# Kernel tuning notes

Measured on AMD Instinct MI355X. Metric: run time of the kernel, lower is better.

## Reference

```python
import jax, jax.numpy as jnp
import numpy as np

L = 4          # dilation_depth
HID = 32       # hidden_channels
F_IN = 16
F_OUT = 16
K = 2          # conv kernel size


def setup_inputs() -> dict:
    key = jax.random.key(0)
    ks = jax.random.split(key, 20)
    B, T, N, F = 8, 512, 128, F_IN
    s = 0.1
    inp = {
        "X": jax.random.normal(ks[0], (B, T, N, F), jnp.float32),
        "A": jax.random.normal(ks[1], (N, N), jnp.float32) / jnp.sqrt(N).astype(jnp.float32),
        "in_w": jax.random.normal(ks[2], (F, 3 * HID), jnp.float32) * s,
        "in_b": jnp.zeros((3 * HID,), jnp.float32),
        "ct_w": jax.random.normal(ks[3], (L, K, HID, HID), jnp.float32) * s,
        "ct_b": jnp.zeros((L, HID), jnp.float32),
        "cs_w": jax.random.normal(ks[4], (L, K, HID, HID), jnp.float32) * s,
        "cs_b": jnp.zeros((L, HID), jnp.float32),
        "gcn_w": jax.random.normal(ks[5], (L, HID, HID), jnp.float32) * s,
        "gcn_b": jnp.zeros((L, HID), jnp.float32),
        "res_w": jax.random.normal(ks[6], (L, HID, HID), jnp.float32) * s,
        "res_b": jnp.zeros((L, HID), jnp.float32),
        "skip_w": jax.random.normal(ks[7], (L, HID, HID), jnp.float32) * s,
        "skip_b": jnp.zeros((L, HID), jnp.float32),
        "out1_w": jax.random.normal(ks[8], (HID, HID), jnp.float32) * s,
        "out1_b": jnp.zeros((HID,), jnp.float32),
        "out2_w": jax.random.normal(ks[9], (HID, F_OUT), jnp.float32) * s,
        "out2_b": jnp.zeros((F_OUT,), jnp.float32),
    }
    return inp


def _causal_conv(x, w, b, dilation):
    # x: [BN, T, C]; w: [K, C_in, C_out] (WIO); causal pad left by dilation*(K-1)
    pad = dilation * (w.shape[0] - 1)
    y = jax.lax.conv_general_dilated(
        x, w, window_strides=(1,), padding=[(pad, 0)],
        rhs_dilation=(dilation,), dimension_numbers=("NWC", "WIO", "NWC"))
    return y + b


def reference(X, A, in_w, in_b, ct_w, ct_b, cs_w, cs_b, gcn_w, gcn_b,
              res_w, res_b, skip_w, skip_b, out1_w, out1_b, out2_w, out2_b):
    B, T, N, F = X.shape
    Xp = X @ in_w + in_b                      # [B,T,N,3H]
    x_a, x_b, x_res = jnp.split(Xp, 3, axis=-1)
    H = x_a.shape[-1]
    # Faithful to source: raw reshape [B,T,N,H] -> [B*N,T,H] (no transpose), as in the original code.
    x_a_r = x_a.reshape(B * N, T, H)
    x_b_r = x_b.reshape(B * N, T, H)
    skip = jnp.zeros_like(x_res)
    for i in range(L):
        d = 2 ** i
        tcn = (jnp.tanh(_causal_conv(x_a_r, ct_w[i], ct_b[i], d))
               * jax.nn.sigmoid(_causal_conv(x_b_r, cs_w[i], cs_b[i], d)))
        tcn = tcn.reshape(B, N, T, H).transpose(0, 2, 1, 3)   # [B,T,N,H]
        gcn = jnp.einsum('ij,btjf->btif', A, x_res) @ gcn_w[i] + gcn_b[i]
        h = tcn + gcn
        x_res = (h @ res_w[i] + res_b[i]) + x_res
        skip = skip + (h @ skip_w[i] + skip_b[i])
    h = jax.nn.relu(skip)
    h = jax.nn.relu(h @ out1_w + out1_b)
    return h @ out2_w + out2_b
```

## Files before the change

### kernel.cpp

```cpp
#include <hip/hip_runtime.h>
#include <math.h>

#define T_ 512

typedef _Float16 half8 __attribute__((ext_vector_type(8)));
typedef _Float16 half4 __attribute__((ext_vector_type(4)));
typedef float f32x4 __attribute__((ext_vector_type(4)));

__device__ __forceinline__ float sigm(float x)  { return 1.0f / (1.0f + __expf(-x)); }
__device__ __forceinline__ float tanhf_(float x){ return 1.0f - 2.0f / (1.0f + __expf(2.0f * x)); }

__device__ __forceinline__ half4 pack4(f32x4 v) {
    half4 h;
    h[0] = (_Float16)v[0]; h[1] = (_Float16)v[1];
    h[2] = (_Float16)v[2]; h[3] = (_Float16)v[3];
    return h;
}

__global__ __launch_bounds__(256) void k_prep(
    const float* __restrict__ A,     const float* __restrict__ in_w,
    const float* __restrict__ in_b,
    const float* __restrict__ ct_w,  const float* __restrict__ ct_b,
    const float* __restrict__ cs_w,  const float* __restrict__ cs_b,
    const float* __restrict__ gcn_w, const float* __restrict__ res_w,
    const float* __restrict__ skip_w,
    const float* __restrict__ out1_w,const float* __restrict__ out2_w,
    _Float16* __restrict__ FR, float* __restrict__ BIAS)
{
    int idx = blockIdx.x * 256 + threadIdx.x;
    if (idx < 16384) {
        int j = idx & 7, L = (idx >> 3) & 63, tile = idx >> 9;
        int it = tile >> 2, kt = tile & 3;
        FR[idx] = (_Float16)A[(it * 16 + (L & 15)) * 128 + kt * 32 + (L >> 4) * 8 + j];
    } else if (idx < 25600) {
        int e = idx - 16384;
        int j = e & 7, L = (e >> 3) & 63, ct = (e >> 9) & 1, mat = e >> 10;
        int k = (L >> 4) * 8 + j, col = ct * 16 + (L & 15);
        float v = 0.f;
        if (mat < 8) {
            int l = mat >> 1, br = mat & 1;
            const float* tw = (br ? cs_w : ct_w) + l * 2048;
            int bro = br * 32;
            if (k < 16) { for (int c = 0; c < 32; ++c) v += in_w[k*96 + bro + c] * tw[c*32 + col]; }
            else        { for (int c = 0; c < 32; ++c) v += in_w[(k-16)*96 + bro + c] * tw[1024 + c*32 + col]; }
        } else {
            v = (k >= 16) ? in_w[(k - 16) * 96 + 64 + col] : 0.f;
        }
        FR[idx] = (_Float16)v;
    } else if (idx < 39936) {
        int e = idx - 25600;
        int i = e & 3, L = (e >> 2) & 63, ct = (e >> 8) & 1, ks = (e >> 9) & 1, mat = e >> 10;
        int k = ks * 16 + (L >> 4) * 4 + i, col = ct * 16 + (L & 15);
        float v;
        if (mat < 12) {
            int l = mat / 3, r = mat - l * 3;
            const float* W = (r == 0) ? gcn_w : (r == 1) ? res_w : skip_w;
            v = W[l * 1024 + k * 32 + col];
        } else if (mat == 12) v = out1_w[k * 32 + col];
        else                  v = (ct == 0) ? out2_w[k * 16 + (L & 15)] : 0.f;
        FR[idx] = (_Float16)v;
    } else if (idx < 40448) {
        int e = idx - 39936;
        int n = e & 31, q = (e >> 5) & 3, l = e >> 7;
        float v = 0.f;
        if (q == 0) { v = ct_b[l*32+n]; for (int c = 0; c < 32; ++c) v += in_b[c]    * ct_w[l*2048 + 1024 + c*32 + n]; }
        else if (q == 1) {              for (int c = 0; c < 32; ++c) v += in_b[c]    * ct_w[l*2048 +        c*32 + n]; }
        else if (q == 2) { v = cs_b[l*32+n]; for (int c = 0; c < 32; ++c) v += in_b[32+c] * cs_w[l*2048 + 1024 + c*32 + n]; }
        else {                          for (int c = 0; c < 32; ++c) v += in_b[32+c] * cs_w[l*2048 +        c*32 + n]; }
        BIAS[l*128 + q*32 + n] = v;
    }
}

__global__ __launch_bounds__(256, 3) void k_fused(
    const float* __restrict__ X,
    const _Float16* __restrict__ FR,
    const float* __restrict__ BIAS,
    const float* __restrict__ in_b,
    const float* __restrict__ gcn_b,
    const float* __restrict__ res_b,
    const float* __restrict__ skip_b,
    const float* __restrict__ b1,
    const float* __restrict__ b2,
    float* __restrict__ out)
{
    __shared__ _Float16 Pld[128 * 40];
    __shared__ _Float16 xsT[2][32 * 136];

    const int btid = blockIdx.x;
    const int b = btid >> 9, t = btid & (T_ - 1);
    const int tid = threadIdx.x, lane = tid & 63, w = tid >> 6;
    const int lm = lane & 15, kb = lane >> 4;
    const int R = w * 32;

    const half8* AFv  = (const half8*)FR;
    const half8* W32v = (const half8*)(FR + 16384);
    const half4* W16v = (const half4*)(FR + 25600);
    const f32x4 zero4 = {0.f, 0.f, 0.f, 0.f};

    const int row = lane >> 1, ch = lane & 1;

    {
        const float4* s4 = (const float4*)(X + ((size_t)btid * 128 + R + row) * 16 + ch * 8);
        float4 u0 = s4[0], u1 = s4[1];
        half8 hv;
        hv[0]=(_Float16)u0.x; hv[1]=(_Float16)u0.y; hv[2]=(_Float16)u0.z; hv[3]=(_Float16)u0.w;
        hv[4]=(_Float16)u1.x; hv[5]=(_Float16)u1.y; hv[6]=(_Float16)u1.z; hv[7]=(_Float16)u1.w;
        half8 z8 = {0,0,0,0,0,0,0,0};
        *(half8*)&Pld[(R + row) * 40 + ch * 8]      = z8;
        *(half8*)&Pld[(R + row) * 40 + 16 + ch * 8] = hv;
    }

    f32x4 xm[2][2], skT[2][2];
    {
        half8 pt0 = *(const half8*)&Pld[(R + lm) * 40 + kb * 8];
        half8 pt1 = *(const half8*)&Pld[(R + 16 + lm) * 40 + kb * 8];
#pragma unroll
        for (int f = 0; f < 2; ++f) {
            half8 wi = W32v[(8 * 2 + f) * 64 + lane];
            float bi = in_b[64 + f * 16 + lm];
            f32x4 d0 = __builtin_amdgcn_mfma_f32_16x16x32_f16(pt0, wi, zero4, 0, 0, 0);
            f32x4 d1 = __builtin_amdgcn_mfma_f32_16x16x32_f16(pt1, wi, zero4, 0, 0, 0);
#pragma unroll
            for (int r = 0; r < 4; ++r) { xm[0][f][r] = d0[r] + bi; xm[1][f][r] = d1[r] + bi; }
        }
#pragma unroll
        for (int a = 0; a < 2; ++a)
#pragma unroll
            for (int c = 0; c < 2; ++c) skT[a][c] = zero4;
    }

    {
        const float4* s4 = (const float4*)(X + ((size_t)(b * 128 + R + row) * T_ + t) * 16 + ch * 8);
        float4 u0 = s4[0], u1 = s4[1];
        half8 hv;
        hv[0]=(_Float16)u0.x; hv[1]=(_Float16)u0.y; hv[2]=(_Float16)u0.z; hv[3]=(_Float16)u0.w;
        hv[4]=(_Float16)u1.x; hv[5]=(_Float16)u1.y; hv[6]=(_Float16)u1.z; hv[7]=(_Float16)u1.w;
        *(half8*)&Pld[(R + row) * 40 + 16 + ch * 8] = hv;
    }

#pragma unroll 1
    for (int l = 0; l < 4; ++l) {
        const int d = 1 << l;
        const bool pv = (t >= d);

        {
            half8 hv = {0,0,0,0,0,0,0,0};
            if (pv) {
                const float4* s4 = (const float4*)(X + ((size_t)(b * 128 + R + row) * T_ + (t - d)) * 16 + ch * 8);
                float4 u0 = s4[0], u1 = s4[1];
                hv[0]=(_Float16)u0.x; hv[1]=(_Float16)u0.y; hv[2]=(_Float16)u0.z; hv[3]=(_Float16)u0.w;
                hv[4]=(_Float16)u1.x; hv[5]=(_Float16)u1.y; hv[6]=(_Float16)u1.z; hv[7]=(_Float16)u1.w;
            }
            *(half8*)&Pld[(R + row) * 40 + ch * 8] = hv;
        }

        half8 pf0 = *(const half8*)&Pld[(R + lm) * 40 + kb * 8];
        half8 pf1 = *(const half8*)&Pld[(R + 16 + lm) * 40 + kb * 8];
        f32x4 tcv[2][2];
#pragma unroll
        for (int ct = 0; ct < 2; ++ct) {
            half8 wt = W32v[((l * 2 + 0) * 2 + ct) * 64 + lane];
            half8 ws = W32v[((l * 2 + 1) * 2 + ct) * 64 + lane];
            f32x4 dt0 = __builtin_amdgcn_mfma_f32_16x16x32_f16(wt, pf0, zero4, 0, 0, 0);
            f32x4 dt1 = __builtin_amdgcn_mfma_f32_16x16x32_f16(wt, pf1, zero4, 0, 0, 0);
            f32x4 ds0 = __builtin_amdgcn_mfma_f32_16x16x32_f16(ws, pf0, zero4, 0, 0, 0);
            f32x4 ds1 = __builtin_amdgcn_mfma_f32_16x16x32_f16(ws, pf1, zero4, 0, 0, 0);
            const float4 bt0 = *(const float4*)&BIAS[l*128 +       ct*16 + kb*4];
            const float4 bt1 = *(const float4*)&BIAS[l*128 + 32 +  ct*16 + kb*4];
            const float4 bs0 = *(const float4*)&BIAS[l*128 + 64 +  ct*16 + kb*4];
            const float4 bs1 = *(const float4*)&BIAS[l*128 + 96 +  ct*16 + kb*4];
            float btq[4] = { bt0.x + (pv ? bt1.x : 0.f), bt0.y + (pv ? bt1.y : 0.f),
                             bt0.z + (pv ? bt1.z : 0.f), bt0.w + (pv ? bt1.w : 0.f) };
            float bsq[4] = { bs0.x + (pv ? bs1.x : 0.f), bs0.y + (pv ? bs1.y : 0.f),
                             bs0.z + (pv ? bs1.z : 0.f), bs0.w + (pv ? bs1.w : 0.f) };
#pragma unroll
            for (int r = 0; r < 4; ++r) {
                tcv[ct][0][r] = tanhf_(dt0[r] + btq[r]) * sigm(ds0[r] + bsq[r]);
                tcv[ct][1][r] = tanhf_(dt1[r] + btq[r]) * sigm(ds1[r] + bsq[r]);
            }
        }

        const int buf = l & 1;
#pragma unroll
        for (int mt = 0; mt < 2; ++mt)
#pragma unroll
            for (int f = 0; f < 2; ++f)
                *(half4*)&xsT[buf][(f * 16 + lm) * 136 + R + mt * 16 + kb * 4] = pack4(xm[mt][f]);
        __syncthreads();

        f32x4 AxT[2][2];
        half8 Afr[2][4];
#pragma unroll
        for (int mt = 0; mt < 2; ++mt)
#pragma unroll
            for (int kt = 0; kt < 4; ++kt)
                Afr[mt][kt] = AFv[((w * 2 + mt) * 4 + kt) * 64 + lane];
#pragma unroll
        for (int f = 0; f < 2; ++f) {
            half8 xa[4];
#pragma unroll
            for (int kt = 0; kt < 4; ++kt)
                xa[kt] = *(const half8*)&xsT[buf][(f * 16 + lm) * 136 + kt * 32 + kb * 8];
#pragma unroll
            for (int mt = 0; mt < 2; ++mt) {
                f32x4 acc = zero4;
#pragma unroll
                for (int kt = 0; kt < 4; ++kt)
                    acc = __builtin_amdgcn_mfma_f32_16x16x32_f16(xa[kt], Afr[mt][kt], acc, 0, 0, 0);
                AxT[f][mt] = acc;
            }
        }

        half4 axh[2][2];
#pragma unroll
        for (int f = 0; f < 2; ++f)
#pragma unroll
            for (int mt = 0; mt < 2; ++mt) axh[f][mt] = pack4(AxT[f][mt]);
        half4 hh[2][2];
#pragma unroll
        for (int g = 0; g < 2; ++g) {
            half4 gw0 = W16v[((l * 3 + 0) * 4 + 0 * 2 + g) * 64 + lane];
            half4 gw1 = W16v[((l * 3 + 0) * 4 + 1 * 2 + g) * 64 + lane];
            const float4 gb = *(const float4*)&gcn_b[l * 32 + g * 16 + kb * 4];
            float gbq[4] = { gb.x, gb.y, gb.z, gb.w };
#pragma unroll
            for (int mt = 0; mt < 2; ++mt) {
                f32x4 acc = __builtin_amdgcn_mfma_f32_16x16x16f16(gw0, axh[0][mt], zero4, 0, 0, 0);
                acc = __builtin_amdgcn_mfma_f32_16x16x16f16(gw1, axh[1][mt], acc, 0, 0, 0);
#pragma unroll
                for (int r = 0; r < 4; ++r) acc[r] += gbq[r] + tcv[g][mt][r];
                hh[g][mt] = pack4(acc);
            }
        }

#pragma unroll
        for (int mt = 0; mt < 2; ++mt)
#pragma unroll
            for (int f3 = 0; f3 < 2; ++f3) {
                half4 rw0 = W16v[((l * 3 + 1) * 4 + 0 * 2 + f3) * 64 + lane];
                half4 rw1 = W16v[((l * 3 + 1) * 4 + 1 * 2 + f3) * 64 + lane];
                f32x4 acc = __builtin_amdgcn_mfma_f32_16x16x16f16(hh[0][mt], rw0, xm[mt][f3], 0, 0, 0);
                xm[mt][f3] = __builtin_amdgcn_mfma_f32_16x16x16f16(hh[1][mt], rw1, acc, 0, 0, 0);
                float rb = res_b[l * 32 + f3 * 16 + lm];
#pragma unroll
                for (int r = 0; r < 4; ++r) xm[mt][f3][r] += rb;

                half4 sw0 = W16v[((l * 3 + 2) * 4 + 0 * 2 + f3) * 64 + lane];
                half4 sw1 = W16v[((l * 3 + 2) * 4 + 1 * 2 + f3) * 64 + lane];
                f32x4 acs = __builtin_amdgcn_mfma_f32_16x16x16f16(sw0, hh[0][mt], skT[f3][mt], 0, 0, 0);
                skT[f3][mt] = __builtin_amdgcn_mfma_f32_16x16x16f16(sw1, hh[1][mt], acs, 0, 0, 0);
                const float4 sb = *(const float4*)&skip_b[l * 32 + f3 * 16 + kb * 4];
                skT[f3][mt][0] += sb.x; skT[f3][mt][1] += sb.y;
                skT[f3][mt][2] += sb.z; skT[f3][mt][3] += sb.w;
            }
    }

    half4 rs[2][2];
#pragma unroll
    for (int g = 0; g < 2; ++g)
#pragma unroll
        for (int mt = 0; mt < 2; ++mt) {
            f32x4 v;
#pragma unroll
            for (int r = 0; r < 4; ++r) v[r] = fmaxf(skT[g][mt][r], 0.f);
            rs[g][mt] = pack4(v);
        }
    half4 h1h[2][2];
#pragma unroll
    for (int g4 = 0; g4 < 2; ++g4) {
        half4 w10 = W16v[(12 * 4 + 0 * 2 + g4) * 64 + lane];
        half4 w11 = W16v[(12 * 4 + 1 * 2 + g4) * 64 + lane];
        const float4 bb = *(const float4*)&b1[g4 * 16 + kb * 4];
        float bbq[4] = { bb.x, bb.y, bb.z, bb.w };
#pragma unroll
        for (int mt = 0; mt < 2; ++mt) {
            f32x4 acc = __builtin_amdgcn_mfma_f32_16x16x16f16(w10, rs[0][mt], zero4, 0, 0, 0);
            acc = __builtin_amdgcn_mfma_f32_16x16x16f16(w11, rs[1][mt], acc, 0, 0, 0);
            f32x4 v;
#pragma unroll
            for (int r = 0; r < 4; ++r) v[r] = fmaxf(acc[r] + bbq[r], 0.f);
            h1h[g4][mt] = pack4(v);
        }
    }
    {
        half4 w20 = W16v[(13 * 4 + 0 * 2 + 0) * 64 + lane];
        half4 w21 = W16v[(13 * 4 + 1 * 2 + 0) * 64 + lane];
        const float4 bb = *(const float4*)&b2[kb * 4];
#pragma unroll
        for (int mt = 0; mt < 2; ++mt) {
            f32x4 acc = __builtin_amdgcn_mfma_f32_16x16x16f16(w20, h1h[0][mt], zero4, 0, 0, 0);
            acc = __builtin_amdgcn_mfma_f32_16x16x16f16(w21, h1h[1][mt], acc, 0, 0, 0);
            float4 o = make_float4(acc[0] + bb.x, acc[1] + bb.y, acc[2] + bb.z, acc[3] + bb.w);
            *(float4*)&out[((size_t)btid * 128 + R + mt * 16 + lm) * 16 + kb * 4] = o;
        }
    }
}

extern "C" void kernel_launch(void* const* d_in, const int* in_sizes, int n_in,
                              void* d_out, int out_size, void* d_ws, size_t ws_size,
                              hipStream_t stream)
{
    const float* X      = (const float*)d_in[0];
    const float* A      = (const float*)d_in[1];
    const float* in_w   = (const float*)d_in[2];
    const float* in_b   = (const float*)d_in[3];
    const float* ct_w   = (const float*)d_in[4];
    const float* ct_b   = (const float*)d_in[5];
    const float* cs_w   = (const float*)d_in[6];
    const float* cs_b   = (const float*)d_in[7];
    const float* gcn_w  = (const float*)d_in[8];
    const float* gcn_b  = (const float*)d_in[9];
    const float* res_w  = (const float*)d_in[10];
    const float* res_b  = (const float*)d_in[11];
    const float* skip_w = (const float*)d_in[12];
    const float* skip_b = (const float*)d_in[13];
    const float* out1_w = (const float*)d_in[14];
    const float* out1_b = (const float*)d_in[15];
    const float* out2_w = (const float*)d_in[16];
    const float* out2_b = (const float*)d_in[17];

    _Float16* FR   = (_Float16*)d_ws;
    float*    BIAS = (float*)((char*)d_ws + 79872);

    k_prep<<<158, 256, 0, stream>>>(A, in_w, in_b, ct_w, ct_b, cs_w, cs_b,
                                    gcn_w, res_w, skip_w, out1_w, out2_w,
                                    FR, BIAS);

    k_fused<<<8 * T_, 256, 0, stream>>>(X, FR, BIAS, in_b,
                                        gcn_b, res_b, skip_b,
                                        out1_b, out2_b, (float*)d_out);
}
```

Before: 240.4 us.

## Fold biases into MFMA accumulators, fuse gated activation, hoist A fragments, remap blocks

Merges tanh*sigmoid into one activation that needs two exps and one reciprocal. Folds the conv, gcn, out1 and out2 biases into the MFMA accumulator init, precomputes the skip bias sum and selects the pv-dependent conv bias per layer. The input projection for x_res now uses a 16x16x16 MFMA with inputs loaded directly from global, so the Pld staging and extra LDS traffic are gone. A fragments are hoisted out of the layer loop, the block index is swizzled across batches, and launch bounds go from 3 to 4 waves per SIMD. The hoisting adds register pressure against the higher occupancy target, and the fused activation may overflow for large inputs.

```diff
diff --git a/kernel.cpp b/kernel.cpp
--- a/kernel.cpp
+++ b/kernel.cpp
@@ -7,8 +7,13 @@
 typedef _Float16 half4 __attribute__((ext_vector_type(4)));
 typedef float f32x4 __attribute__((ext_vector_type(4)));
 
-__device__ __forceinline__ float sigm(float x)  { return 1.0f / (1.0f + __expf(-x)); }
-__device__ __forceinline__ float tanhf_(float x){ return 1.0f - 2.0f / (1.0f + __expf(2.0f * x)); }
+__device__ __forceinline__ float ts_act(float a, float b) {
+    float e2a = __expf(a + a);
+    float eb  = __expf(b);
+    float num = (e2a - 1.0f) * eb;
+    float den = (e2a + 1.0f) * (eb + 1.0f);
+    return num * __builtin_amdgcn_rcpf(den);
+}
 
 __device__ __forceinline__ half4 pack4(f32x4 v) {
     half4 h;
@@ -32,23 +37,19 @@
         int j = idx & 7, L = (idx >> 3) & 63, tile = idx >> 9;
         int it = tile >> 2, kt = tile & 3;
         FR[idx] = (_Float16)A[(it * 16 + (L & 15)) * 128 + kt * 32 + (L >> 4) * 8 + j];
-    } else if (idx < 25600) {
+    } else if (idx < 24576) {
         int e = idx - 16384;
         int j = e & 7, L = (e >> 3) & 63, ct = (e >> 9) & 1, mat = e >> 10;
         int k = (L >> 4) * 8 + j, col = ct * 16 + (L & 15);
+        int l = mat >> 1, br = mat & 1;
+        const float* tw = (br ? cs_w : ct_w) + l * 2048;
+        int bro = br * 32;
         float v = 0.f;
-        if (mat < 8) {
-            int l = mat >> 1, br = mat & 1;
-            const float* tw = (br ? cs_w : ct_w) + l * 2048;
-            int bro = br * 32;
-            if (k < 16) { for (int c = 0; c < 32; ++c) v += in_w[k*96 + bro + c] * tw[c*32 + col]; }
-            else        { for (int c = 0; c < 32; ++c) v += in_w[(k-16)*96 + bro + c] * tw[1024 + c*32 + col]; }
-        } else {
-            v = (k >= 16) ? in_w[(k - 16) * 96 + 64 + col] : 0.f;
-        }
+        if (k < 16) { for (int c = 0; c < 32; ++c) v += in_w[k*96 + bro + c] * tw[c*32 + col]; }
+        else        { for (int c = 0; c < 32; ++c) v += in_w[(k-16)*96 + bro + c] * tw[1024 + c*32 + col]; }
         FR[idx] = (_Float16)v;
     } else if (idx < 39936) {
-        int e = idx - 25600;
+        int e = idx - 24576;
         int i = e & 3, L = (e >> 2) & 63, ct = (e >> 8) & 1, ks = (e >> 9) & 1, mat = e >> 10;
         int k = ks * 16 + (L >> 4) * 4 + i, col = ct * 16 + (L & 15);
         float v;
@@ -57,21 +58,24 @@
             const float* W = (r == 0) ? gcn_w : (r == 1) ? res_w : skip_w;
             v = W[l * 1024 + k * 32 + col];
         } else if (mat == 12) v = out1_w[k * 32 + col];
-        else                  v = (ct == 0) ? out2_w[k * 16 + (L & 15)] : 0.f;
+        else if (mat == 13)   v = (ct == 0) ? out2_w[k * 16 + (L & 15)] : 0.f;
+        else                  v = (ks == 0) ? in_w[k * 96 + 64 + col] : 0.f;
         FR[idx] = (_Float16)v;
     } else if (idx < 40448) {
         int e = idx - 39936;
-        int n = e & 31, q = (e >> 5) & 3, l = e >> 7;
-        float v = 0.f;
-        if (q == 0) { v = ct_b[l*32+n]; for (int c = 0; c < 32; ++c) v += in_b[c]    * ct_w[l*2048 + 1024 + c*32 + n]; }
-        else if (q == 1) {              for (int c = 0; c < 32; ++c) v += in_b[c]    * ct_w[l*2048 +        c*32 + n]; }
-        else if (q == 2) { v = cs_b[l*32+n]; for (int c = 0; c < 32; ++c) v += in_b[32+c] * cs_w[l*2048 + 1024 + c*32 + n]; }
-        else {                          for (int c = 0; c < 32; ++c) v += in_b[32+c] * cs_w[l*2048 +        c*32 + n]; }
-        BIAS[l*128 + q*32 + n] = v;
-    }
-}
-
-__global__ __launch_bounds__(256, 3) void k_fused(
+        int n = e & 31, br = (e >> 5) & 1, pvi = (e >> 6) & 1, l = e >> 7;
+        const float* W  = br ? cs_w : ct_w;
+        const float* bb = br ? cs_b : ct_b;
+        int ibo = br * 32;
+        float v = bb[l * 32 + n];
+        for (int c = 0; c < 32; ++c) v += in_b[ibo + c] * W[l*2048 + 1024 + c*32 + n];
+        if (pvi)
+            for (int c = 0; c < 32; ++c) v += in_b[ibo + c] * W[l*2048 + c*32 + n];
+        BIAS[e] = v;
+    }
+}
+
+__global__ __launch_bounds__(256, 4) void k_fused(
     const float* __restrict__ X,
     const _Float16* __restrict__ FR,
     const float* __restrict__ BIAS,
@@ -86,7 +90,8 @@
     __shared__ _Float16 Pld[128 * 40];
     __shared__ _Float16 xsT[2][32 * 136];
 
-    const int btid = blockIdx.x;
+    const int bx = blockIdx.x;
+    const int btid = ((bx & 7) << 9) | (bx >> 3);
     const int b = btid >> 9, t = btid & (T_ - 1);
     const int tid = threadIdx.x, lane = tid & 63, w = tid >> 6;
     const int lm = lane & 15, kb = lane >> 4;
@@ -94,39 +99,43 @@
 
     const half8* AFv  = (const half8*)FR;
     const half8* W32v = (const half8*)(FR + 16384);
-    const half4* W16v = (const half4*)(FR + 25600);
+    const half4* W16v = (const half4*)(FR + 24576);
     const f32x4 zero4 = {0.f, 0.f, 0.f, 0.f};
 
     const int row = lane >> 1, ch = lane & 1;
 
-    {
-        const float4* s4 = (const float4*)(X + ((size_t)btid * 128 + R + row) * 16 + ch * 8);
-        float4 u0 = s4[0], u1 = s4[1];
-        half8 hv;
-        hv[0]=(_Float16)u0.x; hv[1]=(_Float16)u0.y; hv[2]=(_Float16)u0.z; hv[3]=(_Float16)u0.w;
-        hv[4]=(_Float16)u1.x; hv[5]=(_Float16)u1.y; hv[6]=(_Float16)u1.z; hv[7]=(_Float16)u1.w;
-        half8 z8 = {0,0,0,0,0,0,0,0};
-        *(half8*)&Pld[(R + row) * 40 + ch * 8]      = z8;
-        *(half8*)&Pld[(R + row) * 40 + 16 + ch * 8] = hv;
-    }
+    half8 Afr[2][4];
+#pragma unroll
+    for (int mt = 0; mt < 2; ++mt)
+#pragma unroll
+        for (int kt = 0; kt < 4; ++kt)
+            Afr[mt][kt] = AFv[((w * 2 + mt) * 4 + kt) * 64 + lane];
 
     f32x4 xm[2][2], skT[2][2];
     {
-        half8 pt0 = *(const half8*)&Pld[(R + lm) * 40 + kb * 8];
-        half8 pt1 = *(const half8*)&Pld[(R + 16 + lm) * 40 + kb * 8];
+        const float4 x0 = *(const float4*)(X + ((size_t)btid * 128 + R + lm) * 16 + kb * 4);
+        const float4 x1 = *(const float4*)(X + ((size_t)btid * 128 + R + 16 + lm) * 16 + kb * 4);
+        half4 p0, p1;
+        p0[0]=(_Float16)x0.x; p0[1]=(_Float16)x0.y; p0[2]=(_Float16)x0.z; p0[3]=(_Float16)x0.w;
+        p1[0]=(_Float16)x1.x; p1[1]=(_Float16)x1.y; p1[2]=(_Float16)x1.z; p1[3]=(_Float16)x1.w;
 #pragma unroll
         for (int f = 0; f < 2; ++f) {
-            half8 wi = W32v[(8 * 2 + f) * 64 + lane];
+            half4 wi = W16v[(56 + f) * 64 + lane];
             float bi = in_b[64 + f * 16 + lm];
-            f32x4 d0 = __builtin_amdgcn_mfma_f32_16x16x32_f16(pt0, wi, zero4, 0, 0, 0);
-            f32x4 d1 = __builtin_amdgcn_mfma_f32_16x16x32_f16(pt1, wi, zero4, 0, 0, 0);
-#pragma unroll
-            for (int r = 0; r < 4; ++r) { xm[0][f][r] = d0[r] + bi; xm[1][f][r] = d1[r] + bi; }
-        }
-#pragma unroll
-        for (int a = 0; a < 2; ++a)
-#pragma unroll
-            for (int c = 0; c < 2; ++c) skT[a][c] = zero4;
+            f32x4 cb; cb[0] = bi; cb[1] = bi; cb[2] = bi; cb[3] = bi;
+            xm[0][f] = __builtin_amdgcn_mfma_f32_16x16x16f16(p0, wi, cb, 0, 0, 0);
+            xm[1][f] = __builtin_amdgcn_mfma_f32_16x16x16f16(p1, wi, cb, 0, 0, 0);
+        }
+#pragma unroll
+        for (int f3 = 0; f3 < 2; ++f3) {
+            f32x4 s = zero4;
+#pragma unroll
+            for (int l = 0; l < 4; ++l) {
+                const float4 q = *(const float4*)&skip_b[l * 32 + f3 * 16 + kb * 4];
+                s[0] += q.x; s[1] += q.y; s[2] += q.z; s[3] += q.w;
+            }
+            skT[f3][0] = s; skT[f3][1] = s;
+        }
     }
 
     {
@@ -142,6 +151,7 @@
     for (int l = 0; l < 4; ++l) {
         const int d = 1 << l;
         const bool pv = (t >= d);
+        const float* B2 = BIAS + (l * 2 + (pv ? 1 : 0)) * 64;
 
         {
             half8 hv = {0,0,0,0,0,0,0,0};
@@ -161,22 +171,16 @@
         for (int ct = 0; ct < 2; ++ct) {
             half8 wt = W32v[((l * 2 + 0) * 2 + ct) * 64 + lane];
             half8 ws = W32v[((l * 2 + 1) * 2 + ct) * 64 + lane];
-            f32x4 dt0 = __builtin_amdgcn_mfma_f32_16x16x32_f16(wt, pf0, zero4, 0, 0, 0);
-            f32x4 dt1 = __builtin_amdgcn_mfma_f32_16x16x32_f16(wt, pf1, zero4, 0, 0, 0);
-            f32x4 ds0 = __builtin_amdgcn_mfma_f32_16x16x32_f16(ws, pf0, zero4, 0, 0, 0);
-            f32x4 ds1 = __builtin_amdgcn_mfma_f32_16x16x32_f16(ws, pf1, zero4, 0, 0, 0);
-            const float4 bt0 = *(const float4*)&BIAS[l*128 +       ct*16 + kb*4];
-            const float4 bt1 = *(const float4*)&BIAS[l*128 + 32 +  ct*16 + kb*4];
-            const float4 bs0 = *(const float4*)&BIAS[l*128 + 64 +  ct*16 + kb*4];
-            const float4 bs1 = *(const float4*)&BIAS[l*128 + 96 +  ct*16 + kb*4];
-            float btq[4] = { bt0.x + (pv ? bt1.x : 0.f), bt0.y + (pv ? bt1.y : 0.f),
-                             bt0.z + (pv ? bt1.z : 0.f), bt0.w + (pv ? bt1.w : 0.f) };
-            float bsq[4] = { bs0.x + (pv ? bs1.x : 0.f), bs0.y + (pv ? bs1.y : 0.f),
-                             bs0.z + (pv ? bs1.z : 0.f), bs0.w + (pv ? bs1.w : 0.f) };
+            const f32x4 cT = *(const f32x4*)&B2[ct * 16 + kb * 4];
+            const f32x4 cS = *(const f32x4*)&B2[32 + ct * 16 + kb * 4];
+            f32x4 dt0 = __builtin_amdgcn_mfma_f32_16x16x32_f16(wt, pf0, cT, 0, 0, 0);
+            f32x4 dt1 = __builtin_amdgcn_mfma_f32_16x16x32_f16(wt, pf1, cT, 0, 0, 0);
+            f32x4 ds0 = __builtin_amdgcn_mfma_f32_16x16x32_f16(ws, pf0, cS, 0, 0, 0);
+            f32x4 ds1 = __builtin_amdgcn_mfma_f32_16x16x32_f16(ws, pf1, cS, 0, 0, 0);
 #pragma unroll
             for (int r = 0; r < 4; ++r) {
-                tcv[ct][0][r] = tanhf_(dt0[r] + btq[r]) * sigm(ds0[r] + bsq[r]);
-                tcv[ct][1][r] = tanhf_(dt1[r] + btq[r]) * sigm(ds1[r] + bsq[r]);
+                tcv[ct][0][r] = ts_act(dt0[r], ds0[r]);
+                tcv[ct][1][r] = ts_act(dt1[r], ds1[r]);
             }
         }
 
@@ -189,12 +193,6 @@
         __syncthreads();
 
         f32x4 AxT[2][2];
-        half8 Afr[2][4];
-#pragma unroll
-        for (int mt = 0; mt < 2; ++mt)
-#pragma unroll
-            for (int kt = 0; kt < 4; ++kt)
-                Afr[mt][kt] = AFv[((w * 2 + mt) * 4 + kt) * 64 + lane];
 #pragma unroll
         for (int f = 0; f < 2; ++f) {
             half8 xa[4];
@@ -219,16 +217,15 @@
         half4 hh[2][2];
 #pragma unroll
         for (int g = 0; g < 2; ++g) {
-            half4 gw0 = W16v[((l * 3 + 0) * 4 + 0 * 2 + g) * 64 + lane];
-            half4 gw1 = W16v[((l * 3 + 0) * 4 + 1 * 2 + g) * 64 + lane];
-            const float4 gb = *(const float4*)&gcn_b[l * 32 + g * 16 + kb * 4];
-            float gbq[4] = { gb.x, gb.y, gb.z, gb.w };
+            half4 gw0 = W16v[((l * 3 + 0) * 4 + 0 + g) * 64 + lane];
+            half4 gw1 = W16v[((l * 3 + 0) * 4 + 2 + g) * 64 + lane];
+            const f32x4 gq = *(const f32x4*)&gcn_b[l * 32 + g * 16 + kb * 4];
 #pragma unroll
             for (int mt = 0; mt < 2; ++mt) {
-                f32x4 acc = __builtin_amdgcn_mfma_f32_16x16x16f16(gw0, axh[0][mt], zero4, 0, 0, 0);
+                f32x4 acc = __builtin_amdgcn_mfma_f32_16x16x16f16(gw0, axh[0][mt], gq, 0, 0, 0);
                 acc = __builtin_amdgcn_mfma_f32_16x16x16f16(gw1, axh[1][mt], acc, 0, 0, 0);
 #pragma unroll
-                for (int r = 0; r < 4; ++r) acc[r] += gbq[r] + tcv[g][mt][r];
+                for (int r = 0; r < 4; ++r) acc[r] += tcv[g][mt][r];
                 hh[g][mt] = pack4(acc);
             }
         }
@@ -237,21 +234,18 @@
         for (int mt = 0; mt < 2; ++mt)
 #pragma unroll
             for (int f3 = 0; f3 < 2; ++f3) {
-                half4 rw0 = W16v[((l * 3 + 1) * 4 + 0 * 2 + f3) * 64 + lane];
-                half4 rw1 = W16v[((l * 3 + 1) * 4 + 1 * 2 + f3) * 64 + lane];
+                half4 rw0 = W16v[((l * 3 + 1) * 4 + 0 + f3) * 64 + lane];
+                half4 rw1 = W16v[((l * 3 + 1) * 4 + 2 + f3) * 64 + lane];
                 f32x4 acc = __builtin_amdgcn_mfma_f32_16x16x16f16(hh[0][mt], rw0, xm[mt][f3], 0, 0, 0);
                 xm[mt][f3] = __builtin_amdgcn_mfma_f32_16x16x16f16(hh[1][mt], rw1, acc, 0, 0, 0);
                 float rb = res_b[l * 32 + f3 * 16 + lm];
 #pragma unroll
                 for (int r = 0; r < 4; ++r) xm[mt][f3][r] += rb;
 
-                half4 sw0 = W16v[((l * 3 + 2) * 4 + 0 * 2 + f3) * 64 + lane];
-                half4 sw1 = W16v[((l * 3 + 2) * 4 + 1 * 2 + f3) * 64 + lane];
+                half4 sw0 = W16v[((l * 3 + 2) * 4 + 0 + f3) * 64 + lane];
+                half4 sw1 = W16v[((l * 3 + 2) * 4 + 2 + f3) * 64 + lane];
                 f32x4 acs = __builtin_amdgcn_mfma_f32_16x16x16f16(sw0, hh[0][mt], skT[f3][mt], 0, 0, 0);
                 skT[f3][mt] = __builtin_amdgcn_mfma_f32_16x16x16f16(sw1, hh[1][mt], acs, 0, 0, 0);
-                const float4 sb = *(const float4*)&skip_b[l * 32 + f3 * 16 + kb * 4];
-                skT[f3][mt][0] += sb.x; skT[f3][mt][1] += sb.y;
-                skT[f3][mt][2] += sb.z; skT[f3][mt][3] += sb.w;
             }
     }
 
@@ -268,29 +262,28 @@
     half4 h1h[2][2];
 #pragma unroll
     for (int g4 = 0; g4 < 2; ++g4) {
-        half4 w10 = W16v[(12 * 4 + 0 * 2 + g4) * 64 + lane];
-        half4 w11 = W16v[(12 * 4 + 1 * 2 + g4) * 64 + lane];
-        const float4 bb = *(const float4*)&b1[g4 * 16 + kb * 4];
-        float bbq[4] = { bb.x, bb.y, bb.z, bb.w };
+        half4 w10 = W16v[(48 + 0 + g4) * 64 + lane];
+        half4 w11 = W16v[(48 + 2 + g4) * 64 + lane];
+        const f32x4 bq = *(const f32x4*)&b1[g4 * 16 + kb * 4];
 #pragma unroll
         for (int mt = 0; mt < 2; ++mt) {
-            f32x4 acc = __builtin_amdgcn_mfma_f32_16x16x16f16(w10, rs[0][mt], zero4, 0, 0, 0);
+            f32x4 acc = __builtin_amdgcn_mfma_f32_16x16x16f16(w10, rs[0][mt], bq, 0, 0, 0);
             acc = __builtin_amdgcn_mfma_f32_16x16x16f16(w11, rs[1][mt], acc, 0, 0, 0);
             f32x4 v;
 #pragma unroll
-            for (int r = 0; r < 4; ++r) v[r] = fmaxf(acc[r] + bbq[r], 0.f);
+            for (int r = 0; r < 4; ++r) v[r] = fmaxf(acc[r], 0.f);
             h1h[g4][mt] = pack4(v);
         }
     }
     {
-        half4 w20 = W16v[(13 * 4 + 0 * 2 + 0) * 64 + lane];
-        half4 w21 = W16v[(13 * 4 + 1 * 2 + 0) * 64 + lane];
-        const float4 bb = *(const float4*)&b2[kb * 4];
+        half4 w20 = W16v[(52 + 0) * 64 + lane];
+        half4 w21 = W16v[(52 + 2) * 64 + lane];
+        const f32x4 b2q = *(const f32x4*)&b2[kb * 4];
 #pragma unroll
         for (int mt = 0; mt < 2; ++mt) {
-            f32x4 acc = __builtin_amdgcn_mfma_f32_16x16x16f16(w20, h1h[0][mt], zero4, 0, 0, 0);
+            f32x4 acc = __builtin_amdgcn_mfma_f32_16x16x16f16(w20, h1h[0][mt], b2q, 0, 0, 0);
             acc = __builtin_amdgcn_mfma_f32_16x16x16f16(w21, h1h[1][mt], acc, 0, 0, 0);
-            float4 o = make_float4(acc[0] + bb.x, acc[1] + bb.y, acc[2] + bb.z, acc[3] + bb.w);
+            float4 o = make_float4(acc[0], acc[1], acc[2], acc[3]);
             *(float4*)&out[((size_t)btid * 128 + R + mt * 16 + lm) * 16 + kb * 4] = o;
         }
     }
```

Result: slower. 272.7 us (+13.5%).
